# Optimization experiments

Measured on AMD Instinct MI355X. Metric: run time of the kernel, lower is better.

The kernel has to match this reference:

```python
import jax, jax.numpy as jnp
import numpy as np

NUM_HEADS = 16

def setup_inputs() -> dict:
    key = jax.random.key(0)
    k1, k2, k3 = jax.random.split(key, 3)
    T, B, E = 2048, 4, 1024
    x = jax.random.normal(k1, (T, B, E), dtype=jnp.float32)
    # xavier-ish scale for weights
    in_proj_w = jax.random.normal(k2, (3 * E, E), dtype=jnp.float32) * (1.0 / np.sqrt(E))
    in_proj_b = jnp.zeros((3 * E,), dtype=jnp.float32)
    out_w = jax.random.normal(k3, (E, E), dtype=jnp.float32) * (1.0 / np.sqrt(E))
    out_b = jnp.zeros((E,), dtype=jnp.float32)
    return {"x": x, "in_proj_w": in_proj_w, "in_proj_b": in_proj_b, "out_w": out_w, "out_b": out_b}

def reference(x, in_proj_w, in_proj_b, out_w, out_b):
    # Self-attention (qkv_same path), dropout=0, eval mode, no masks.
    T, B, E = x.shape
    H = NUM_HEADS
    Dh = E // H
    scaling = Dh ** (-0.5)
    # fused in-projection: [T,B,3E]
    qkv = jnp.einsum('tbe,fe->tbf', x, in_proj_w) + in_proj_b
    q, k, v = jnp.split(qkv, 3, axis=-1)
    q = q * scaling
    # [T,B,E] -> [B,H,T,Dh]
    def to_heads(t):
        return t.reshape(T, B, H, Dh).transpose(1, 2, 0, 3)
    q, k, v = to_heads(q), to_heads(k), to_heads(v)
    # full TxT score matrix, softmax in float32 (matches F.softmax(..., dtype=float32))
    scores = jnp.einsum('bhtd,bhsd->bhts', q, k)
    attn_weights = jax.nn.softmax(scores.astype(jnp.float32), axis=-1).astype(scores.dtype)
    attn = jnp.einsum('bhts,bhsd->bhtd', attn_weights, v)
    # [B,H,T,Dh] -> [T,B,E]
    attn = attn.transpose(2, 0, 1, 3).reshape(T, B, E)
    attn = jnp.einsum('tbe,fe->tbf', attn, out_w) + out_b
    # need_weights=True: average over heads -> [B,T,T]
    avg_weights = attn_weights.sum(axis=1) / H
    return attn, avg_weights
```

## Files before the change

### kernel.cpp

```cpp
#include <hip/hip_runtime.h>
#include <stdint.h>

#define DEV __device__ __forceinline__

typedef __attribute__((ext_vector_type(8))) __bf16 bf16x8;
typedef __attribute__((ext_vector_type(4))) __bf16 bf16x4;
typedef __attribute__((ext_vector_type(4))) float f32x4;

DEV unsigned short f2bf(float f){
  union { float fv; unsigned u; } v; v.fv = f;
  unsigned r = v.u + 0x7fffu + ((v.u >> 16) & 1u);
  return (unsigned short)(r >> 16);
}

DEV void gload16(const void* g, void* l){
  __builtin_amdgcn_global_load_lds((const __attribute__((address_space(1))) void*)g,
                                   (__attribute__((address_space(3))) void*)l,
                                   16, 0, 0);
}

__global__ void k_cvt(const float* __restrict__ src, unsigned short* __restrict__ dst){
  const int i = (blockIdx.x * blockDim.x + threadIdx.x) << 2;
  const float4 v = *(const float4*)(src + i);
  ushort4 o;
  o.x = f2bf(v.x); o.y = f2bf(v.y); o.z = f2bf(v.z); o.w = f2bf(v.w);
  *(ushort4*)(dst + i) = o;
}

template<int MODE>
__launch_bounds__(256)
__global__ void k_gemm(const unsigned short* __restrict__ A,
                       const unsigned short* __restrict__ Bm,
                       const float* __restrict__ bias,
                       float* __restrict__ outF,
                       unsigned short* __restrict__ Qm,
                       unsigned short* __restrict__ Km,
                       unsigned short* __restrict__ VTm)
{
  __shared__ unsigned short As[128*64];
  __shared__ unsigned short Bs[128*64];
  const int tid  = threadIdx.x;
  const int lane = tid & 63;
  const int wid  = tid >> 6;
  const int wr   = wid >> 1;
  const int wc   = wid & 1;
  const int wg = blockIdx.x;
  int bx, by;
  if (MODE == 0){ const int slot = wg >> 3; bx = (wg & 7) + 8*(slot >> 6); by = slot & 63; }
  else          { bx = wg & 7; by = wg >> 3; }
  const int r0   = by * 128;
  const int c0   = bx * 128;
  const int l15  = lane & 15;
  const int l4   = lane >> 4;

  f32x4 acc[4][4];
#pragma unroll
  for (int m = 0; m < 4; ++m)
#pragma unroll
    for (int n = 0; n < 4; ++n)
      acc[m][n] = (f32x4){0.f, 0.f, 0.f, 0.f};

  for (int k0 = 0; k0 < 1024; k0 += 64){
#pragma unroll
    for (int i = 0; i < 4; ++i){
      const int sb   = (i*4 + wid)*64;
      const int slot = sb + lane;
      const int row  = slot >> 3;
      const int cg   = (slot & 7) ^ (row & 7);
      gload16(A  + (size_t)(r0 + row)*1024 + k0 + cg*8, (void*)(As + sb*8));
      gload16(Bm + (size_t)(c0 + row)*1024 + k0 + cg*8, (void*)(Bs + sb*8));
    }
    __syncthreads();
#pragma unroll
    for (int kk = 0; kk < 2; ++kk){
      bf16x8 af[4], bf[4];
#pragma unroll
      for (int m = 0; m < 4; ++m){
        const int row = wr*64 + m*16 + l15;
        const int ch  = (kk*4 + l4) ^ (row & 7);
        af[m] = *(const bf16x8*)(As + row*64 + ch*8);
      }
#pragma unroll
      for (int n = 0; n < 4; ++n){
        const int row = wc*64 + n*16 + l15;
        const int ch  = (kk*4 + l4) ^ (row & 7);
        bf[n] = *(const bf16x8*)(Bs + row*64 + ch*8);
      }
#pragma unroll
      for (int m = 0; m < 4; ++m)
#pragma unroll
        for (int n = 0; n < 4; ++n)
          acc[m][n] = __builtin_amdgcn_mfma_f32_16x16x32_bf16(af[m], bf[n], acc[m][n], 0, 0, 0);
    }
    __syncthreads();
  }

  if (MODE == 0){
#pragma unroll
    for (int n = 0; n < 4; ++n){
      const int f     = c0 + wc*64 + n*16 + l15;
      const float bs  = bias[f];
      const int which = f >> 10;
      const int fi    = f & 1023;
      const int h     = fi >> 6;
      const int d     = fi & 63;
#pragma unroll
      for (int m = 0; m < 4; ++m){
        const int rb = r0 + wr*64 + m*16 + (l4 << 2);
#pragma unroll
        for (int j = 0; j < 4; ++j){
          const int r = rb + j;
          const int t = r >> 2;
          const int b = r & 3;
          float v = acc[m][n][j] + bs;
          if (which == 0) v *= 0.18033688f;
          const unsigned short bv = f2bf(v);
          const int bh = b*16 + h;
          if (which == 0)      Qm [((size_t)bh*2048 + t)*64 + d] = bv;
          else if (which == 1) Km [((size_t)bh*2048 + t)*64 + d] = bv;
          else                 VTm[((size_t)bh*64 + d)*2048 + t] = bv;
        }
      }
    }
  } else {
#pragma unroll
    for (int m = 0; m < 4; ++m){
      const int rb = r0 + wr*64 + m*16 + (l4 << 2);
#pragma unroll
      for (int n = 0; n < 4; ++n){
        const int f    = c0 + wc*64 + n*16 + l15;
        const float bs = bias[f];
#pragma unroll
        for (int j = 0; j < 4; ++j)
          outF[(size_t)(rb + j)*1024 + f] = acc[m][n][j] + bs;
      }
    }
  }
}

__launch_bounds__(512)
__global__ void k_pv(const unsigned short* __restrict__ Qm,
                     const unsigned short* __restrict__ Km,
                     const unsigned short* __restrict__ VTm,
                     float* __restrict__ linv,
                     unsigned short* __restrict__ ctx)
{
  __shared__ unsigned short Ws[128*64];
  __shared__ unsigned short Ks[2][64*64];
  __shared__ unsigned short Vs[2][64*64];
  const int tid = threadIdx.x, lane = tid & 63, wid = tid >> 6;
  const int l15 = lane & 15, l4 = lane >> 4;
  const int wg = blockIdx.x;
  const int slotb = wg >> 3;
  const int bh = (wg & 7) + 8*(slotb >> 4);
  const int t0 = (slotb & 15) * 128;
  const unsigned short* Qb = Qm  + (size_t)bh*131072;
  const unsigned short* Kb = Km  + (size_t)bh*131072;
  const unsigned short* Vb = VTm + (size_t)bh*131072;

  {
    const int slot = tid;
    const int row = slot >> 3;
    const int cg = (slot & 7) ^ (row & 7);
    gload16(Kb + (size_t)row*64 + cg*8, (void*)(Ks[0] + slot*8));
    gload16(Vb + (size_t)row*2048 + cg*8, (void*)(Vs[0] + slot*8));
  }
  bf16x8 aq[2];
#pragma unroll
  for (int kk = 0; kk < 2; ++kk)
    aq[kk] = *(const bf16x8*)(Qb + (size_t)(t0 + wid*16 + l15)*64 + (kk*4 + l4)*8);
  __syncthreads();

  f32x4 oacc[4];
#pragma unroll
  for (int n = 0; n < 4; ++n) oacc[n] = (f32x4){0.f,0.f,0.f,0.f};
  float lacc = 0.f;

  const int wrow = wid*16 + l15;
  const int rx   = l15 & 7;

  for (int s0 = 0; s0 < 2048; s0 += 64){
    const int cur = (s0 >> 6) & 1;
    if (s0 + 64 < 2048){
      const int slot = tid;
      const int row = slot >> 3;
      const int cg = (slot & 7) ^ (row & 7);
      gload16(Kb + (size_t)(s0 + 64 + row)*64 + cg*8, (void*)(Ks[cur^1] + slot*8));
      gload16(Vb + (size_t)row*2048 + (s0 + 64) + cg*8, (void*)(Vs[cur^1] + slot*8));
    }
#pragma unroll
    for (int n = 0; n < 4; ++n){
      f32x4 sacc = (f32x4){0.f,0.f,0.f,0.f};
#pragma unroll
      for (int kk = 0; kk < 2; ++kk){
        const int sr = n*16 + l15;
        const int ch = (kk*4 + l4) ^ (sr & 7);
        const bf16x8 ak = *(const bf16x8*)(Ks[cur] + sr*64 + ch*8);
        sacc = __builtin_amdgcn_mfma_f32_16x16x32_bf16(ak, aq[kk], sacc, 0, 0, 0);
      }
      f32x4 pv;
      pv[0] = __builtin_amdgcn_exp2f(sacc[0]);
      pv[1] = __builtin_amdgcn_exp2f(sacc[1]);
      pv[2] = __builtin_amdgcn_exp2f(sacc[2]);
      pv[3] = __builtin_amdgcn_exp2f(sacc[3]);
      lacc += (pv[0] + pv[1]) + (pv[2] + pv[3]);
      const bf16x4 pb = __builtin_convertvector(pv, bf16x4);
      const int g = (n*4 + l4) ^ (rx << 1);
      *(bf16x4*)(Ws + wrow*64 + g*4) = pb;
    }
    bf16x8 aw[2];
#pragma unroll
    for (int kk = 0; kk < 2; ++kk){
      const int c = (kk*4 + l4) ^ rx;
      aw[kk] = *(const bf16x8*)(Ws + wrow*64 + c*8);
    }
#pragma unroll
    for (int n = 0; n < 4; ++n){
#pragma unroll
      for (int kk = 0; kk < 2; ++kk){
        const int dr = n*16 + l15;
        const int ch = (kk*4 + l4) ^ (dr & 7);
        const bf16x8 bv = *(const bf16x8*)(Vs[cur] + dr*64 + ch*8);
        oacc[n] = __builtin_amdgcn_mfma_f32_16x16x32_bf16(aw[kk], bv, oacc[n], 0, 0, 0);
      }
    }
    __syncthreads();
  }

  lacc += __shfl_xor(lacc, 16);
  lacc += __shfl_xor(lacc, 32);
  const float rl = 1.0f / lacc;
  if (lane < 16)
    linv[(size_t)bh*2048 + t0 + wid*16 + lane] = rl;

  float rlj[4];
#pragma unroll
  for (int j = 0; j < 4; ++j)
    rlj[j] = __shfl(rl, (l4 << 2) + j);

  const int b = bh >> 4, h = bh & 15;
#pragma unroll
  for (int n = 0; n < 4; ++n){
#pragma unroll
    for (int j = 0; j < 4; ++j){
      const int t = t0 + wid*16 + (l4 << 2) + j;
      const int d = n*16 + l15;
      ctx[((size_t)t*4 + b)*1024 + h*64 + d] = f2bf(oacc[n][j] * rlj[j]);
    }
  }
}

__launch_bounds__(256)
__global__ void k_avg(const unsigned short* __restrict__ Qm,
                      const unsigned short* __restrict__ Km,
                      const float* __restrict__ linv,
                      float* __restrict__ avg)
{
  __shared__ unsigned short Ks[2][128*64];
  const int tid = threadIdx.x, lane = tid & 63, wid = tid >> 6;
  const int l15 = lane & 15, l4 = lane >> 4;
  const int wg = blockIdx.x;
  const int slotb = wg >> 3;
  const int combo = (wg & 7) + 8*(slotb >> 5);
  const int b   = combo >> 4;
  const int s0  = (combo & 15) * 128;
  const int t0  = (slotb & 31) * 64;

  float wacc[8][4];
#pragma unroll
  for (int n = 0; n < 8; ++n)
#pragma unroll
    for (int j = 0; j < 4; ++j) wacc[n][j] = 0.f;

  {
    const unsigned short* Kb = Km + (size_t)(b*16)*131072;
#pragma unroll
    for (int i = 0; i < 4; ++i){
      const int slot = i*256 + tid;
      const int row = slot >> 3;
      const int cg = (slot & 7) ^ (row & 7);
      gload16(Kb + (size_t)(s0 + row)*64 + cg*8, (void*)(Ks[0] + slot*8));
    }
  }
  __syncthreads();

  for (int h = 0; h < 16; ++h){
    const int cur = h & 1;
    if (h < 15){
      const unsigned short* Kb = Km + (size_t)(b*16 + h + 1)*131072;
#pragma unroll
      for (int i = 0; i < 4; ++i){
        const int slot = i*256 + tid;
        const int row = slot >> 3;
        const int cg = (slot & 7) ^ (row & 7);
        gload16(Kb + (size_t)(s0 + row)*64 + cg*8, (void*)(Ks[cur^1] + slot*8));
      }
    }
    const int bh = b*16 + h;
    const unsigned short* Qb = Qm + (size_t)bh*131072;

    bf16x8 aq[2];
#pragma unroll
    for (int kk = 0; kk < 2; ++kk)
      aq[kk] = *(const bf16x8*)(Qb + (size_t)(t0 + wid*16 + l15)*64 + (kk*4 + l4)*8);

    float4 lj = *(const float4*)(linv + (size_t)bh*2048 + t0 + wid*16 + (l4 << 2));
    lj.x *= 0.0625f; lj.y *= 0.0625f; lj.z *= 0.0625f; lj.w *= 0.0625f;

#pragma unroll
    for (int n = 0; n < 8; ++n){
      f32x4 sacc = (f32x4){0.f,0.f,0.f,0.f};
#pragma unroll
      for (int kk = 0; kk < 2; ++kk){
        const int row = n*16 + l15;
        const int ch  = (kk*4 + l4) ^ (row & 7);
        const bf16x8 bk = *(const bf16x8*)(Ks[cur] + row*64 + ch*8);
        sacc = __builtin_amdgcn_mfma_f32_16x16x32_bf16(aq[kk], bk, sacc, 0, 0, 0);
      }
      wacc[n][0] += __builtin_amdgcn_exp2f(sacc[0]) * lj.x;
      wacc[n][1] += __builtin_amdgcn_exp2f(sacc[1]) * lj.y;
      wacc[n][2] += __builtin_amdgcn_exp2f(sacc[2]) * lj.z;
      wacc[n][3] += __builtin_amdgcn_exp2f(sacc[3]) * lj.w;
    }
    __syncthreads();
  }

#pragma unroll
  for (int n = 0; n < 8; ++n)
#pragma unroll
    for (int j = 0; j < 4; ++j){
      const int t = t0 + wid*16 + (l4 << 2) + j;
      const int s = s0 + n*16 + l15;
      avg[((size_t)b*2048 + t)*2048 + s] = wacc[n][j];
    }
}

extern "C" void kernel_launch(void* const* d_in, const int* in_sizes, int n_in,
                              void* d_out, int out_size, void* d_ws, size_t ws_size,
                              hipStream_t stream)
{
  const float* x    = (const float*)d_in[0];
  const float* wqkv = (const float*)d_in[1];
  const float* bqkv = (const float*)d_in[2];
  const float* wout = (const float*)d_in[3];
  const float* bout = (const float*)d_in[4];
  float* out = (float*)d_out;

  char* ws = (char*)d_ws;
  unsigned short* xb    = (unsigned short*)(ws);
  unsigned short* wqkvb = (unsigned short*)(ws + ((size_t)16 << 20));
  unsigned short* woutb = (unsigned short*)(ws + ((size_t)24 << 20));
  unsigned short* Qm    = (unsigned short*)(ws + ((size_t)26 << 20));
  unsigned short* Km    = (unsigned short*)(ws + ((size_t)42 << 20));
  unsigned short* VTm   = (unsigned short*)(ws + ((size_t)58 << 20));
  unsigned short* ctx   = (unsigned short*)(ws + ((size_t)74 << 20));
  float* linv = (float*)(ws + ((size_t)90 << 20));

  k_cvt<<<8192, 256, 0, stream>>>(x,    xb);
  k_cvt<<<3072, 256, 0, stream>>>(wqkv, wqkvb);
  k_cvt<<<1024, 256, 0, stream>>>(wout, woutb);

  k_gemm<0><<<1536, 256, 0, stream>>>(xb, wqkvb, bqkv, nullptr, Qm, Km, VTm);
  k_pv     <<<1024, 512, 0, stream>>>(Qm, Km, VTm, linv, ctx);
  k_avg    <<<2048, 256, 0, stream>>>(Qm, Km, linv, out + 8388608);
  k_gemm<1><<< 512, 256, 0, stream>>>(ctx, woutb, bout, out, nullptr, nullptr, nullptr);
}
```

Before: 299.4 us.

## Give each PV-kernel warp two query sub-tiles to reuse K/V fragments

The attention PV kernel now runs 256 threads per block instead of 512, and each warp handles 32 query rows (two 16-row sub-tiles) instead of 16. Each K and V fragment read from shared memory feeds two MFMAs, which halves LDS reads per MFMA. Each thread now issues two global-to-LDS loads per tile. The cost is more accumulator registers per thread and half as many warps per block to hide latency.

```diff
diff --git a/kernel.cpp b/kernel.cpp
--- a/kernel.cpp
+++ b/kernel.cpp
@@ -138,7 +138,7 @@
   }
 }
 
-__launch_bounds__(512)
+__launch_bounds__(256)
 __global__ void k_pv(const unsigned short* __restrict__ Qm,
                      const unsigned short* __restrict__ Km,
                      const unsigned short* __restrict__ VTm,
@@ -158,94 +158,109 @@
   const unsigned short* Kb = Km  + (size_t)bh*131072;
   const unsigned short* Vb = VTm + (size_t)bh*131072;
 
-  {
-    const int slot = tid;
+#pragma unroll
+  for (int i = 0; i < 2; ++i){
+    const int slot = i*256 + tid;
     const int row = slot >> 3;
     const int cg = (slot & 7) ^ (row & 7);
     gload16(Kb + (size_t)row*64 + cg*8, (void*)(Ks[0] + slot*8));
     gload16(Vb + (size_t)row*2048 + cg*8, (void*)(Vs[0] + slot*8));
   }
-  bf16x8 aq[2];
-#pragma unroll
-  for (int kk = 0; kk < 2; ++kk)
-    aq[kk] = *(const bf16x8*)(Qb + (size_t)(t0 + wid*16 + l15)*64 + (kk*4 + l4)*8);
+  bf16x8 aq[2][2];
+#pragma unroll
+  for (int qs = 0; qs < 2; ++qs)
+#pragma unroll
+    for (int kk = 0; kk < 2; ++kk)
+      aq[qs][kk] = *(const bf16x8*)(Qb + (size_t)(t0 + wid*32 + qs*16 + l15)*64 + (kk*4 + l4)*8);
   __syncthreads();
 
-  f32x4 oacc[4];
-#pragma unroll
-  for (int n = 0; n < 4; ++n) oacc[n] = (f32x4){0.f,0.f,0.f,0.f};
-  float lacc = 0.f;
-
-  const int wrow = wid*16 + l15;
-  const int rx   = l15 & 7;
+  f32x4 oacc[2][4];
+#pragma unroll
+  for (int qs = 0; qs < 2; ++qs)
+#pragma unroll
+    for (int n = 0; n < 4; ++n) oacc[qs][n] = (f32x4){0.f,0.f,0.f,0.f};
+  float lacc[2] = {0.f, 0.f};
+  const int rx = l15 & 7;
 
   for (int s0 = 0; s0 < 2048; s0 += 64){
     const int cur = (s0 >> 6) & 1;
     if (s0 + 64 < 2048){
-      const int slot = tid;
-      const int row = slot >> 3;
-      const int cg = (slot & 7) ^ (row & 7);
-      gload16(Kb + (size_t)(s0 + 64 + row)*64 + cg*8, (void*)(Ks[cur^1] + slot*8));
-      gload16(Vb + (size_t)row*2048 + (s0 + 64) + cg*8, (void*)(Vs[cur^1] + slot*8));
+#pragma unroll
+      for (int i = 0; i < 2; ++i){
+        const int slot = i*256 + tid;
+        const int row = slot >> 3;
+        const int cg = (slot & 7) ^ (row & 7);
+        gload16(Kb + (size_t)(s0 + 64 + row)*64 + cg*8, (void*)(Ks[cur^1] + slot*8));
+        gload16(Vb + (size_t)row*2048 + (s0 + 64) + cg*8, (void*)(Vs[cur^1] + slot*8));
+      }
     }
 #pragma unroll
     for (int n = 0; n < 4; ++n){
-      f32x4 sacc = (f32x4){0.f,0.f,0.f,0.f};
+      bf16x8 ak[2];
 #pragma unroll
       for (int kk = 0; kk < 2; ++kk){
-        const int sr = n*16 + l15;
-        const int ch = (kk*4 + l4) ^ (sr & 7);
-        const bf16x8 ak = *(const bf16x8*)(Ks[cur] + sr*64 + ch*8);
-        sacc = __builtin_amdgcn_mfma_f32_16x16x32_bf16(ak, aq[kk], sacc, 0, 0, 0);
-      }
-      f32x4 pv;
-      pv[0] = __builtin_amdgcn_exp2f(sacc[0]);
-      pv[1] = __builtin_amdgcn_exp2f(sacc[1]);
-      pv[2] = __builtin_amdgcn_exp2f(sacc[2]);
-      pv[3] = __builtin_amdgcn_exp2f(sacc[3]);
-      lacc += (pv[0] + pv[1]) + (pv[2] + pv[3]);
-      const bf16x4 pb = __builtin_convertvector(pv, bf16x4);
-      const int g = (n*4 + l4) ^ (rx << 1);
-      *(bf16x4*)(Ws + wrow*64 + g*4) = pb;
-    }
-    bf16x8 aw[2];
-#pragma unroll
-    for (int kk = 0; kk < 2; ++kk){
-      const int c = (kk*4 + l4) ^ rx;
-      aw[kk] = *(const bf16x8*)(Ws + wrow*64 + c*8);
-    }
+        const int ch = (kk*4 + l4) ^ rx;
+        ak[kk] = *(const bf16x8*)(Ks[cur] + (n*16 + l15)*64 + ch*8);
+      }
+#pragma unroll
+      for (int qs = 0; qs < 2; ++qs){
+        f32x4 sacc = (f32x4){0.f,0.f,0.f,0.f};
+        sacc = __builtin_amdgcn_mfma_f32_16x16x32_bf16(ak[0], aq[qs][0], sacc, 0, 0, 0);
+        sacc = __builtin_amdgcn_mfma_f32_16x16x32_bf16(ak[1], aq[qs][1], sacc, 0, 0, 0);
+        f32x4 pv;
+        pv[0] = __builtin_amdgcn_exp2f(sacc[0]);
+        pv[1] = __builtin_amdgcn_exp2f(sacc[1]);
+        pv[2] = __builtin_amdgcn_exp2f(sacc[2]);
+        pv[3] = __builtin_amdgcn_exp2f(sacc[3]);
+        lacc[qs] += (pv[0] + pv[1]) + (pv[2] + pv[3]);
+        const bf16x4 pb = __builtin_convertvector(pv, bf16x4);
+        const int wrow = wid*32 + qs*16 + l15;
+        const int g = (n*4 + l4) ^ (rx << 1);
+        *(bf16x4*)(Ws + wrow*64 + g*4) = pb;
+      }
+    }
+    bf16x8 aw[2][2];
+#pragma unroll
+    for (int qs = 0; qs < 2; ++qs)
+#pragma unroll
+      for (int kk = 0; kk < 2; ++kk){
+        const int c = (kk*4 + l4) ^ rx;
+        aw[qs][kk] = *(const bf16x8*)(Ws + (wid*32 + qs*16 + l15)*64 + c*8);
+      }
 #pragma unroll
     for (int n = 0; n < 4; ++n){
 #pragma unroll
       for (int kk = 0; kk < 2; ++kk){
-        const int dr = n*16 + l15;
-        const int ch = (kk*4 + l4) ^ (dr & 7);
-        const bf16x8 bv = *(const bf16x8*)(Vs[cur] + dr*64 + ch*8);
-        oacc[n] = __builtin_amdgcn_mfma_f32_16x16x32_bf16(aw[kk], bv, oacc[n], 0, 0, 0);
+        const int ch = (kk*4 + l4) ^ rx;
+        const bf16x8 bv = *(const bf16x8*)(Vs[cur] + (n*16 + l15)*64 + ch*8);
+#pragma unroll
+        for (int qs = 0; qs < 2; ++qs)
+          oacc[qs][n] = __builtin_amdgcn_mfma_f32_16x16x32_bf16(aw[qs][kk], bv, oacc[qs][n], 0, 0, 0);
       }
     }
     __syncthreads();
   }
 
-  lacc += __shfl_xor(lacc, 16);
-  lacc += __shfl_xor(lacc, 32);
-  const float rl = 1.0f / lacc;
-  if (lane < 16)
-    linv[(size_t)bh*2048 + t0 + wid*16 + lane] = rl;
-
-  float rlj[4];
-#pragma unroll
-  for (int j = 0; j < 4; ++j)
-    rlj[j] = __shfl(rl, (l4 << 2) + j);
-
   const int b = bh >> 4, h = bh & 15;
 #pragma unroll
-  for (int n = 0; n < 4; ++n){
-#pragma unroll
-    for (int j = 0; j < 4; ++j){
-      const int t = t0 + wid*16 + (l4 << 2) + j;
-      const int d = n*16 + l15;
-      ctx[((size_t)t*4 + b)*1024 + h*64 + d] = f2bf(oacc[n][j] * rlj[j]);
+  for (int qs = 0; qs < 2; ++qs){
+    lacc[qs] += __shfl_xor(lacc[qs], 16);
+    lacc[qs] += __shfl_xor(lacc[qs], 32);
+    const float rl = 1.0f / lacc[qs];
+    if (lane < 16)
+      linv[(size_t)bh*2048 + t0 + wid*32 + qs*16 + lane] = rl;
+    float rlj[4];
+#pragma unroll
+    for (int j = 0; j < 4; ++j)
+      rlj[j] = __shfl(rl, (l4 << 2) + j);
+#pragma unroll
+    for (int n = 0; n < 4; ++n){
+#pragma unroll
+      for (int j = 0; j < 4; ++j){
+        const int t = t0 + wid*32 + qs*16 + (l4 << 2) + j;
+        const int d = n*16 + l15;
+        ctx[((size_t)t*4 + b)*1024 + h*64 + d] = f2bf(oacc[qs][n][j] * rlj[j]);
+      }
     }
   }
 }
@@ -361,7 +376,7 @@
   k_cvt<<<1024, 256, 0, stream>>>(wout, woutb);
 
   k_gemm<0><<<1536, 256, 0, stream>>>(xb, wqkvb, bqkv, nullptr, Qm, Km, VTm);
-  k_pv     <<<1024, 512, 0, stream>>>(Qm, Km, VTm, linv, ctx);
+  k_pv     <<<1024, 256, 0, stream>>>(Qm, Km, VTm, linv, ctx);
   k_avg    <<<2048, 256, 0, stream>>>(Qm, Km, linv, out + 8388608);
   k_gemm<1><<< 512, 256, 0, stream>>>(ctx, woutb, bout, out, nullptr, nullptr, nullptr);
 }
```

After: 306.3 us. 2.3% more time.
